# Optimization experiments

Hardware: AMD Instinct MI355X
Metric: run time of the kernel (lower is better)

Reference implementation:

```python
import jax, jax.numpy as jnp
import numpy as np

T, D, DFF = 8192, 512, 2048
EPS = 1e-5
LS_INIT = 1e-4

def setup_inputs() -> dict:
    key = jax.random.key(0)
    ks = jax.random.split(key, 5)
    s = 0.02
    return {
        "x": jax.random.normal(ks[0], (T, D), jnp.float32),
        "W_in": jax.random.normal(ks[1], (3 * D, D), jnp.float32) * s,
        "W_out": jax.random.normal(ks[2], (D, D), jnp.float32) * s,
        "W1": jax.random.normal(ks[3], (DFF, D), jnp.float32) * s,
        "W2": jax.random.normal(ks[4], (D, DFF), jnp.float32) * s,
        "g1": jnp.ones((D,), jnp.float32),
        "b1": jnp.zeros((D,), jnp.float32),
        "g2": jnp.ones((D,), jnp.float32),
        "b2": jnp.zeros((D,), jnp.float32),
        "ls1": jnp.full((D,), LS_INIT, jnp.float32),
        "ls2": jnp.full((D,), LS_INIT, jnp.float32),
    }

def _layer_norm(x, g, b):
    mu = jnp.mean(x, axis=-1, keepdims=True)
    var = jnp.mean((x - mu) ** 2, axis=-1, keepdims=True)
    return (x - mu) * jax.lax.rsqrt(var + EPS) * g + b

def reference(x, W_in, W_out, W1, W2, g1, b1, g2, b2, ls1, ls2):
    t = x.shape[0]
    # --- self-attention block (faithful: no head split, no 1/sqrt(d) scale, k @ q^T) ---
    h = _layer_norm(x, g1, b1)                       # [T, D]
    proj = h @ W_in.T                                # [T, 3D]
    q, k, v = jnp.split(proj, 3, axis=-1)            # each [T, D]
    scores = k @ q.T                                 # [T, T]
    mask = jnp.tril(jnp.ones((t, t), scores.dtype))
    scores = jnp.where(mask == 0, -jnp.inf, scores)
    attn = jax.nn.softmax(scores, axis=-1)
    o = (attn @ v) @ W_out.T                         # [T, D]
    x = x + ls1 * o
    # --- FFN block ---
    h = _layer_norm(x, g2, b2)
    update = jax.nn.gelu(h @ W1.T) @ W2.T            # [T, D]
    return x + ls2 * update
```

## Files before the change

kernel.cpp:

```cpp
#include <hip/hip_runtime.h>
#include <hip/hip_bf16.h>


using bf16 = __hip_bfloat16;
typedef __attribute__((ext_vector_type(8))) short short8;
typedef __attribute__((ext_vector_type(4))) float f32x4;

#define T_DIM 8192

#define AS1C(p) (const __attribute__((address_space(1))) void*)(p)
#define AS3P(p) (__attribute__((address_space(3))) void*)(p)
#define GLL16(src, dst) __builtin_amdgcn_global_load_lds(AS1C(src), AS3P(dst), 16, 0, 0)

static __device__ __forceinline__ short f2bfbits(float f) {
  bf16 b = __float2bfloat16(f);
  short s; __builtin_memcpy(&s, &b, 2); return s;
}
static __device__ __forceinline__ float bfbits2f(short s) {
  unsigned u = ((unsigned)(unsigned short)s) << 16;
  float f; __builtin_memcpy(&f, &u, 4); return f;
}

__global__ void cvt4_kernel(
    const float* __restrict__ a, bf16* __restrict__ oa, int na,
    const float* __restrict__ b, bf16* __restrict__ ob, int nb,
    const float* __restrict__ c, bf16* __restrict__ oc, int nc,
    const float* __restrict__ d, bf16* __restrict__ od, int nd)
{
  int i = blockIdx.x * 256 + threadIdx.x;
  if (i < na) { oa[i] = __float2bfloat16(a[i]); return; }
  i -= na;
  if (i < nb) { ob[i] = __float2bfloat16(b[i]); return; }
  i -= nb;
  if (i < nc) { oc[i] = __float2bfloat16(c[i]); return; }
  i -= nc;
  if (i < nd) od[i] = __float2bfloat16(d[i]);
}

__global__ __launch_bounds__(256) void ln_kernel(
    const float* __restrict__ x, const float* __restrict__ g,
    const float* __restrict__ bb, bf16* __restrict__ h)
{
  const int row = blockIdx.x * 4 + (threadIdx.x >> 6);
  const int lane = threadIdx.x & 63;
  const float* xr = x + (size_t)row * 512 + lane * 8;
  f32x4 v0 = *(const f32x4*)xr;
  f32x4 v1 = *(const f32x4*)(xr + 4);
  float s = 0.f;
#pragma unroll
  for (int j = 0; j < 4; ++j) s += v0[j] + v1[j];
#pragma unroll
  for (int d = 1; d < 64; d <<= 1) s += __shfl_xor(s, d);
  const float mu = s * (1.f / 512.f);
  float vs = 0.f;
#pragma unroll
  for (int j = 0; j < 4; ++j) { float a = v0[j] - mu, b2 = v1[j] - mu; vs += a * a + b2 * b2; }
#pragma unroll
  for (int d = 1; d < 64; d <<= 1) vs += __shfl_xor(vs, d);
  const float rs = rsqrtf(vs * (1.f / 512.f) + 1e-5f);
  const f32x4 g0 = *(const f32x4*)(g + lane * 8);
  const f32x4 g1v = *(const f32x4*)(g + lane * 8 + 4);
  const f32x4 b0 = *(const f32x4*)(bb + lane * 8);
  const f32x4 b1v = *(const f32x4*)(bb + lane * 8 + 4);
  short8 ov;
#pragma unroll
  for (int j = 0; j < 4; ++j) {
    ov[j]     = f2bfbits((v0[j] - mu) * rs * g0[j] + b0[j]);
    ov[j + 4] = f2bfbits((v1[j] - mu) * rs * g1v[j] + b1v[j]);
  }
  *(short8*)(h + (size_t)row * 512 + lane * 8) = ov;
}

enum { MODE_BF16 = 0, MODE_GELU = 1, MODE_RESID = 2 };

static __device__ __forceinline__ float gelu_f(float x) {
  float x3 = x * x * x;
  float t = tanhf(0.7978845608028654f * (x + 0.044715f * x3));
  return 0.5f * x * (1.0f + t);
}

template <int MODE>
__global__ __launch_bounds__(256, 2) void gemm_bt(
    const bf16* __restrict__ A, const bf16* __restrict__ B,
    int M, int N, int K,
    bf16* __restrict__ Cb, float* __restrict__ Cf,
    const float* __restrict__ resid, const float* __restrict__ scale)
{
  __shared__ bf16 sA[128 * 64];
  __shared__ bf16 sB[128 * 64];
  const int tid = threadIdx.x;
  const int lane = tid & 63, wave = tid >> 6;
  const int bm = blockIdx.x, bn = blockIdx.y;
  const int wm = (wave & 1) * 64, wn = (wave >> 1) * 64;
  const int ln = lane & 15, lg = lane >> 4;
  f32x4 acc[4][4] = {};

  const int nkt = K >> 6;
  for (int kt = 0; kt < nkt; ++kt) {
    __syncthreads();
#pragma unroll
    for (int r = 0; r < 4; ++r) {
      const int s = r * 256 + tid;
      const int ks = s >> 9, rb = (s >> 6) & 7, l = s & 63;
      const bf16* srcA = A + (size_t)(bm * 128 + rb * 16 + (l & 15)) * K + kt * 64 + ks * 32 + (l >> 4) * 8;
      GLL16(srcA, sA + (size_t)(r * 256 + wave * 64) * 8);
      const bf16* srcB = B + (size_t)(bn * 128 + rb * 16 + (l & 15)) * K + kt * 64 + ks * 32 + (l >> 4) * 8;
      GLL16(srcB, sB + (size_t)(r * 256 + wave * 64) * 8);
    }
    __syncthreads();
#pragma unroll
    for (int ks = 0; ks < 2; ++ks) {
      short8 af[4], bfr[4];
#pragma unroll
      for (int mi = 0; mi < 4; ++mi)
        af[mi] = *(const short8*)(sA + (size_t)(ks * 512 + ((wm >> 4) + mi) * 64 + lane) * 8);
#pragma unroll
      for (int ni = 0; ni < 4; ++ni)
        bfr[ni] = *(const short8*)(sB + (size_t)(ks * 512 + ((wn >> 4) + ni) * 64 + lane) * 8);
#pragma unroll
      for (int mi = 0; mi < 4; ++mi)
#pragma unroll
        for (int ni = 0; ni < 4; ++ni)
          acc[mi][ni] = __builtin_amdgcn_mfma_f32_16x16x32_bf16(af[mi], bfr[ni], acc[mi][ni], 0, 0, 0);
    }
  }
#pragma unroll
  for (int mi = 0; mi < 4; ++mi) {
#pragma unroll
    for (int ni = 0; ni < 4; ++ni) {
#pragma unroll
      for (int r = 0; r < 4; ++r) {
        const int row = bm * 128 + wm + mi * 16 + lg * 4 + r;
        const int col = bn * 128 + wn + ni * 16 + ln;
        const size_t idx = (size_t)row * N + col;
        float v = acc[mi][ni][r];
        if constexpr (MODE == MODE_GELU) { Cb[idx] = __float2bfloat16(gelu_f(v)); }
        else if constexpr (MODE == MODE_RESID) { Cf[idx] = resid[idx] + scale[col] * v; }
        else { Cb[idx] = __float2bfloat16(v); }
      }
    }
  }
}

__global__ __launch_bounds__(256) void transpose_v(const bf16* __restrict__ proj, bf16* __restrict__ vT) {
  __shared__ bf16 tile[64][66];
  const int t0 = blockIdx.x * 64, d0 = blockIdx.y * 64;
  const int tid = threadIdx.x;
#pragma unroll
  for (int i = 0; i < 16; ++i) {
    const int lin = i * 256 + tid;
    const int r = lin >> 6, c = lin & 63;
    tile[r][c] = proj[(size_t)(t0 + r) * 1536 + 1024 + d0 + c];
  }
  __syncthreads();
#pragma unroll
  for (int i = 0; i < 16; ++i) {
    const int lin = i * 256 + tid;
    const int dy = lin >> 6, tx = lin & 63;
    vT[(size_t)(d0 + dy) * T_DIM + t0 + tx] = tile[tx][dy];
  }
}

__global__ __launch_bounds__(512, 2) void attn_kernel(
    const bf16* __restrict__ proj, const bf16* __restrict__ vT,
    bf16* __restrict__ Op, float* __restrict__ mlp)
{
  __shared__ bf16 sQ[2][32 * 512];
  __shared__ bf16 sV[2][32 * 512];
  __shared__ bf16 sP[8][16 * 40];

  const int tid = threadIdx.x, lane = tid & 63, wave = tid >> 6;
  const int ln = lane & 15, lg = lane >> 4;
  const int b = 511 - blockIdx.x;
  const int it = b >> 3;
  const int ch = b & 7;
  const int nj = 4 * it + 4;
  const int jlo = ch * nj / 8;
  const int jhi = (ch + 1) * nj / 8;
  const int wrow = it * 128 + wave * 16;

  short8 kf[16];
#pragma unroll
  for (int ks = 0; ks < 16; ++ks)
    kf[ks] = *(const short8*)(proj + (size_t)(wrow + ln) * 1536 + 512 + ks * 32 + lg * 8);

  f32x4 oa[32] = {};
  float m_r[4] = {-__builtin_inff(), -__builtin_inff(), -__builtin_inff(), -__builtin_inff()};
  float l_r[4] = {0.f, 0.f, 0.f, 0.f};

  auto stageQ = [&](int c, int jt) {
    const int j0 = jt * 32;
#pragma unroll
    for (int r = 0; r < 4; ++r) {
      const int s = r * 512 + tid;
      const int l = s & 63;
      const int ks = s >> 7, jb = (s >> 6) & 1;
      const bf16* srcQ = proj + (size_t)(j0 + jb * 16 + (l & 15)) * 1536 + ks * 32 + (l >> 4) * 8;
      GLL16(srcQ, &sQ[c][(size_t)(r * 512 + wave * 64) * 8]);
    }
  };
  auto stageV = [&](int c, int jt) {
    const int j0 = jt * 32;
#pragma unroll
    for (int r = 0; r < 4; ++r) {
      const int s = r * 512 + tid;
      const int l = s & 63;
      const int nb = s >> 6;
      const bf16* srcV = vT + (size_t)(nb * 16 + (l & 15)) * T_DIM + j0 + (l >> 4) * 8;
      GLL16(srcV, &sV[c][(size_t)(r * 512 + wave * 64) * 8]);
    }
  };

  if (jlo < jhi) {
    int cur = 0;
    stageQ(0, jlo);
    stageV(0, jlo);
    for (int jt = jlo; jt < jhi; ++jt) {
      const int j0 = jt * 32;
      const bool more = (jt + 1 < jhi);
      if (more) stageQ(cur ^ 1, jt + 1);
      if (more) { asm volatile("s_waitcnt vmcnt(8)" ::: "memory"); }
      else      { asm volatile("s_waitcnt vmcnt(4)" ::: "memory"); }
      __builtin_amdgcn_s_barrier();
      __builtin_amdgcn_sched_barrier(0);
      if (j0 <= wrow + 15) {
        f32x4 sfr[2] = {};
        __builtin_amdgcn_s_setprio(1);
#pragma unroll
        for (int ks = 0; ks < 16; ++ks) {
          short8 q0 = *(const short8*)(&sQ[cur][(size_t)(ks * 128 + lane) * 8]);
          short8 q1 = *(const short8*)(&sQ[cur][(size_t)(ks * 128 + 64 + lane) * 8]);
          sfr[0] = __builtin_amdgcn_mfma_f32_16x16x32_bf16(kf[ks], q0, sfr[0], 0, 0, 0);
          sfr[1] = __builtin_amdgcn_mfma_f32_16x16x32_bf16(kf[ks], q1, sfr[1], 0, 0, 0);
        }
        __builtin_amdgcn_s_setprio(0);
        if (j0 + 31 > wrow) {
#pragma unroll
          for (int jb = 0; jb < 2; ++jb)
#pragma unroll
            for (int r = 0; r < 4; ++r) {
              const int i = wrow + lg * 4 + r, j = j0 + jb * 16 + ln;
              if (j > i) sfr[jb][r] = -__builtin_inff();
            }
        }
        float mx[4], sc[4], mm[4];
#pragma unroll
        for (int r = 0; r < 4; ++r) mx[r] = fmaxf(sfr[0][r], sfr[1][r]);
#pragma unroll
        for (int d = 1; d < 16; d <<= 1)
#pragma unroll
          for (int r = 0; r < 4; ++r) mx[r] = fmaxf(mx[r], __shfl_xor(mx[r], d));
#pragma unroll
        for (int r = 0; r < 4; ++r) {
          mm[r] = fmaxf(fmaxf(m_r[r], mx[r]), -1e30f);
          sc[r] = __expf(m_r[r] - mm[r]);
          m_r[r] = mm[r];
          l_r[r] *= sc[r];
        }
        float ts[4] = {0.f, 0.f, 0.f, 0.f};
#pragma unroll
        for (int jb = 0; jb < 2; ++jb)
#pragma unroll
          for (int r = 0; r < 4; ++r) {
            float p = __expf(sfr[jb][r] - mm[r]);
            sfr[jb][r] = p;
            ts[r] += p;
          }
#pragma unroll
        for (int d = 1; d < 16; d <<= 1)
#pragma unroll
          for (int r = 0; r < 4; ++r) ts[r] += __shfl_xor(ts[r], d);
#pragma unroll
        for (int r = 0; r < 4; ++r) l_r[r] += ts[r];
#pragma unroll
        for (int jb = 0; jb < 2; ++jb)
#pragma unroll
          for (int r = 0; r < 4; ++r)
            sP[wave][(lg * 4 + r) * 40 + jb * 16 + ln] = __float2bfloat16(sfr[jb][r]);
#pragma unroll
        for (int nb = 0; nb < 32; ++nb)
#pragma unroll
          for (int r = 0; r < 4; ++r) oa[nb][r] *= sc[r];
      }
      if (more) stageV(cur ^ 1, jt + 1);
      if (more) { asm volatile("s_waitcnt vmcnt(8)" ::: "memory"); }
      else      { asm volatile("s_waitcnt vmcnt(0)" ::: "memory"); }
      __builtin_amdgcn_s_barrier();
      __builtin_amdgcn_sched_barrier(0);
      if (j0 <= wrow + 15) {
        const short8 pa = *(const short8*)(&sP[wave][0] + ln * 40 + lg * 8);
        __builtin_amdgcn_s_setprio(1);
#define LDV(nb) (*(const short8*)(&sV[cur][(size_t)((nb) * 64 + lane) * 8]))
        short8 vf0 = LDV(0), vf1 = LDV(1), vf2 = LDV(2), vf3 = LDV(3);
#pragma unroll
        for (int nb = 0; nb < 28; nb += 4) {
          const short8 w0 = vf0, w1 = vf1, w2 = vf2, w3 = vf3;
          vf0 = LDV(nb + 4); vf1 = LDV(nb + 5); vf2 = LDV(nb + 6); vf3 = LDV(nb + 7);
          oa[nb]     = __builtin_amdgcn_mfma_f32_16x16x32_bf16(pa, w0, oa[nb],     0, 0, 0);
          oa[nb + 1] = __builtin_amdgcn_mfma_f32_16x16x32_bf16(pa, w1, oa[nb + 1], 0, 0, 0);
          oa[nb + 2] = __builtin_amdgcn_mfma_f32_16x16x32_bf16(pa, w2, oa[nb + 2], 0, 0, 0);
          oa[nb + 3] = __builtin_amdgcn_mfma_f32_16x16x32_bf16(pa, w3, oa[nb + 3], 0, 0, 0);
        }
        oa[28] = __builtin_amdgcn_mfma_f32_16x16x32_bf16(pa, vf0, oa[28], 0, 0, 0);
        oa[29] = __builtin_amdgcn_mfma_f32_16x16x32_bf16(pa, vf1, oa[29], 0, 0, 0);
        oa[30] = __builtin_amdgcn_mfma_f32_16x16x32_bf16(pa, vf2, oa[30], 0, 0, 0);
        oa[31] = __builtin_amdgcn_mfma_f32_16x16x32_bf16(pa, vf3, oa[31], 0, 0, 0);
#undef LDV
        __builtin_amdgcn_s_setprio(0);
      }
      cur ^= 1;
    }
  }
#pragma unroll
  for (int nb = 0; nb < 32; ++nb)
#pragma unroll
    for (int r = 0; r < 4; ++r)
      Op[((size_t)ch * T_DIM + wrow + lg * 4 + r) * 512 + nb * 16 + ln] = __float2bfloat16(oa[nb][r]);
  if (ln == 0) {
#pragma unroll
    for (int r = 0; r < 4; ++r) {
      mlp[((size_t)ch * T_DIM + wrow + lg * 4 + r) * 2 + 0] = m_r[r];
      mlp[((size_t)ch * T_DIM + wrow + lg * 4 + r) * 2 + 1] = l_r[r];
    }
  }
}

__global__ __launch_bounds__(256) void combine_kernel(
    const bf16* __restrict__ Op, const float* __restrict__ mlp, bf16* __restrict__ o)
{
  const int row = blockIdx.x * 4 + (threadIdx.x >> 6);
  const int lane = threadIdx.x & 63;
  const int k = 8;
  float m = -__builtin_inff();
  for (int c = 0; c < k; ++c) m = fmaxf(m, mlp[((size_t)c * T_DIM + row) * 2]);
  float l = 0.f;
  for (int c = 0; c < k; ++c) {
    const float mc = mlp[((size_t)c * T_DIM + row) * 2];
    const float lc = mlp[((size_t)c * T_DIM + row) * 2 + 1];
    l += __expf(mc - m) * lc;
  }
  const float inv = 1.0f / l;
  f32x4 a0 = {}, a1 = {};
  for (int c = 0; c < k; ++c) {
    const float w = __expf(mlp[((size_t)c * T_DIM + row) * 2] - m);
    const short8 u = *(const short8*)(Op + ((size_t)c * T_DIM + row) * 512 + lane * 8);
#pragma unroll
    for (int j = 0; j < 4; ++j) {
      a0[j] += w * bfbits2f(u[j]);
      a1[j] += w * bfbits2f(u[j + 4]);
    }
  }
  short8 ov;
#pragma unroll
  for (int j = 0; j < 4; ++j) {
    ov[j]     = f2bfbits(a0[j] * inv);
    ov[j + 4] = f2bfbits(a1[j] * inv);
  }
  *(short8*)(o + (size_t)row * 512 + lane * 8) = ov;
}

extern "C" void kernel_launch(void* const* d_in, const int* in_sizes, int n_in,
                              void* d_out, int out_size, void* d_ws, size_t ws_size,
                              hipStream_t stream) {
  (void)in_sizes; (void)n_in; (void)out_size; (void)ws_size;
  const float* x    = (const float*)d_in[0];
  const float* Win  = (const float*)d_in[1];
  const float* Wout = (const float*)d_in[2];
  const float* W1   = (const float*)d_in[3];
  const float* W2   = (const float*)d_in[4];
  const float* g1   = (const float*)d_in[5];
  const float* b1   = (const float*)d_in[6];
  const float* g2   = (const float*)d_in[7];
  const float* b2   = (const float*)d_in[8];
  const float* ls1  = (const float*)d_in[9];
  const float* ls2  = (const float*)d_in[10];
  float* out = (float*)d_out;

  char* w = (char*)d_ws;
  size_t off = 0;
  auto alloc = [&](size_t bytes) -> char* {
    char* p = w + off; off += (bytes + 255) & ~(size_t)255; return p;
  };
  bf16* wWin  = (bf16*)alloc((size_t)1536 * 512 * 2);
  bf16* wWout = (bf16*)alloc((size_t)512 * 512 * 2);
  bf16* wW1   = (bf16*)alloc((size_t)2048 * 512 * 2);
  bf16* wW2   = (bf16*)alloc((size_t)512 * 2048 * 2);
  bf16* h     = (bf16*)alloc((size_t)T_DIM * 512 * 2);
  bf16* proj  = (bf16*)alloc((size_t)T_DIM * 1536 * 2);
  bf16* vTb   = (bf16*)alloc((size_t)512 * T_DIM * 2);
  bf16* o     = (bf16*)alloc((size_t)T_DIM * 512 * 2);
  float* x1   = (float*)alloc((size_t)T_DIM * 512 * 4);
  bf16* Op    = (bf16*)alloc((size_t)8 * T_DIM * 512 * 2);
  float* mlp  = (float*)alloc((size_t)8 * T_DIM * 2 * 4);
  bf16* f1 = proj;

  cvt4_kernel<<<(1536 * 512 + 512 * 512 + 2048 * 512 + 512 * 2048 + 255) / 256, 256, 0, stream>>>(
      Win, wWin, 1536 * 512, Wout, wWout, 512 * 512,
      W1, wW1, 2048 * 512, W2, wW2, 512 * 2048);

  ln_kernel<<<T_DIM / 4, 256, 0, stream>>>(x, g1, b1, h);
  gemm_bt<MODE_BF16><<<dim3(64, 12), 256, 0, stream>>>(h, wWin, 8192, 1536, 512, proj, nullptr, nullptr, nullptr);
  transpose_v<<<dim3(T_DIM / 64, 8), 256, 0, stream>>>(proj, vTb);
  attn_kernel<<<512, 512, 0, stream>>>(proj, vTb, Op, mlp);
  combine_kernel<<<T_DIM / 4, 256, 0, stream>>>(Op, mlp, o);
  gemm_bt<MODE_RESID><<<dim3(64, 4), 256, 0, stream>>>(o, wWout, 8192, 512, 512, nullptr, x1, x, ls1);
  ln_kernel<<<T_DIM / 4, 256, 0, stream>>>(x1, g2, b2, h);
  gemm_bt<MODE_GELU><<<dim3(64, 16), 256, 0, stream>>>(h, wW1, 8192, 2048, 512, f1, nullptr, nullptr, nullptr);
  gemm_bt<MODE_RESID><<<dim3(64, 4), 256, 0, stream>>>(f1, wW2, 8192, 512, 2048, nullptr, out, x1, ls2);
}
```

Baseline: 329.1 us.

## Double-buffer LDS tiles in bf16 GEMM to overlap global loads with MFMA

The GEMM kernel now keeps two LDS buffers for the A and B tiles and issues the asynchronous global-to-LDS loads for the next k-tile before computing on the current one. It waits on a partial vmcnt so only the current tile's loads must be complete. It also raises wave priority around the MFMA block. This aims to hide global memory latency behind matrix math. The cost is twice the LDS use, which may reduce occupancy, and it relies on correct waitcnt accounting for the asynchronous loads.

```diff
diff --git a/kernel.cpp b/kernel.cpp
--- a/kernel.cpp
+++ b/kernel.cpp
@@ -86,8 +86,8 @@
     bf16* __restrict__ Cb, float* __restrict__ Cf,
     const float* __restrict__ resid, const float* __restrict__ scale)
 {
-  __shared__ bf16 sA[128 * 64];
-  __shared__ bf16 sB[128 * 64];
+  __shared__ bf16 sA[2][128 * 64];
+  __shared__ bf16 sB[2][128 * 64];
   const int tid = threadIdx.x;
   const int lane = tid & 63, wave = tid >> 6;
   const int bm = blockIdx.x, bn = blockIdx.y;
@@ -95,34 +95,50 @@
   const int ln = lane & 15, lg = lane >> 4;
   f32x4 acc[4][4] = {};
 
-  const int nkt = K >> 6;
-  for (int kt = 0; kt < nkt; ++kt) {
-    __syncthreads();
+  auto stage = [&](int c, int kt) {
 #pragma unroll
     for (int r = 0; r < 4; ++r) {
       const int s = r * 256 + tid;
       const int ks = s >> 9, rb = (s >> 6) & 7, l = s & 63;
       const bf16* srcA = A + (size_t)(bm * 128 + rb * 16 + (l & 15)) * K + kt * 64 + ks * 32 + (l >> 4) * 8;
-      GLL16(srcA, sA + (size_t)(r * 256 + wave * 64) * 8);
+      GLL16(srcA, &sA[c][(size_t)(r * 256 + wave * 64) * 8]);
       const bf16* srcB = B + (size_t)(bn * 128 + rb * 16 + (l & 15)) * K + kt * 64 + ks * 32 + (l >> 4) * 8;
-      GLL16(srcB, sB + (size_t)(r * 256 + wave * 64) * 8);
-    }
-    __syncthreads();
+      GLL16(srcB, &sB[c][(size_t)(r * 256 + wave * 64) * 8]);
+    }
+  };
+
+  const int nkt = K >> 6;
+  int cur = 0;
+  stage(0, 0);
+  for (int kt = 0; kt < nkt; ++kt) {
+    if (kt + 1 < nkt) {
+      stage(cur ^ 1, kt + 1);
+      asm volatile("s_waitcnt vmcnt(8)" ::: "memory");
+    } else {
+      asm volatile("s_waitcnt vmcnt(0)" ::: "memory");
+    }
+    __builtin_amdgcn_s_barrier();
+    __builtin_amdgcn_sched_barrier(0);
 #pragma unroll
     for (int ks = 0; ks < 2; ++ks) {
       short8 af[4], bfr[4];
 #pragma unroll
       for (int mi = 0; mi < 4; ++mi)
-        af[mi] = *(const short8*)(sA + (size_t)(ks * 512 + ((wm >> 4) + mi) * 64 + lane) * 8);
+        af[mi] = *(const short8*)(&sA[cur][(size_t)(ks * 512 + ((wm >> 4) + mi) * 64 + lane) * 8]);
 #pragma unroll
       for (int ni = 0; ni < 4; ++ni)
-        bfr[ni] = *(const short8*)(sB + (size_t)(ks * 512 + ((wn >> 4) + ni) * 64 + lane) * 8);
+        bfr[ni] = *(const short8*)(&sB[cur][(size_t)(ks * 512 + ((wn >> 4) + ni) * 64 + lane) * 8]);
+      __builtin_amdgcn_s_setprio(1);
 #pragma unroll
       for (int mi = 0; mi < 4; ++mi)
 #pragma unroll
         for (int ni = 0; ni < 4; ++ni)
           acc[mi][ni] = __builtin_amdgcn_mfma_f32_16x16x32_bf16(af[mi], bfr[ni], acc[mi][ni], 0, 0, 0);
-    }
+      __builtin_amdgcn_s_setprio(0);
+    }
+    __builtin_amdgcn_s_barrier();
+    __builtin_amdgcn_sched_barrier(0);
+    cur ^= 1;
   }
 #pragma unroll
   for (int mi = 0; mi < 4; ++mi) {
```

Measured after the change: 336.5 us. 2.3% more time.
